# Kernel optimization log

Measured on AMD Instinct MI355X. Metric: run time of the kernel, lower is better.

## Reference

```python
import jax, jax.numpy as jnp
import numpy as np

B, D = 200000, 128
K = 1024


def setup_inputs() -> dict:
    key = jax.random.key(0)
    k1, k2 = jax.random.split(key)
    x_BD = jax.random.normal(k1, (B, D), dtype=jnp.float32)
    codebook = jax.random.uniform(k2, (K, D), dtype=jnp.float32)
    return {"x_BD": x_BD, "codebook": codebook}


def reference(x_BD, codebook):
    x_sq_B1 = jnp.sum(x_BD * x_BD, axis=-1, keepdims=True)
    c_sq_K = jnp.sum(codebook * codebook, axis=-1)
    dists_BK = x_sq_B1 - 2.0 * jnp.einsum("bd,kd->bk", x_BD, codebook) + c_sq_K
    codes_B = jnp.argmin(dists_BK, axis=-1)  # [B] int
    quant_x_BD = codebook[codes_B]           # gather, [B, D]
    return quant_x_BD, codes_B
```

## Files before the change

### kernel.cpp

```cpp
#include <hip/hip_runtime.h>


typedef float v2f __attribute__((ext_vector_type(2)));

#define DDIM 128
#define KCODES 1024
#define BM 64
#define BN 128
#define DCH 32
#define NTILES (KCODES / BN)
#define NCHUNK (DDIM / DCH)

__global__ void csq_kernel(const float* __restrict__ cb, float* __restrict__ csq) {
    int k = blockIdx.x * blockDim.x + threadIdx.x;
    if (k >= KCODES) return;
    const float* __restrict__ c = cb + (long)k * DDIM;
    float s0 = 0.f, s1 = 0.f, s2 = 0.f, s3 = 0.f;
#pragma unroll
    for (int d = 0; d < DDIM; d += 4) {
        s0 = fmaf(c[d + 0], c[d + 0], s0);
        s1 = fmaf(c[d + 1], c[d + 1], s1);
        s2 = fmaf(c[d + 2], c[d + 2], s2);
        s3 = fmaf(c[d + 3], c[d + 3], s3);
    }
    csq[k] = (s0 + s1) + (s2 + s3);
}

__launch_bounds__(256, 3)
__global__ void vq_gemm_kernel(const float* __restrict__ x, const float* __restrict__ cb,
                               const float* __restrict__ csq, float* __restrict__ quant,
                               float* __restrict__ codes) {
    __shared__ float xs[DDIM * BM];
    __shared__ float cs[DCH * BN];
    __shared__ int win[BM];

    const int tid = threadIdx.x;
    const long r0 = (long)blockIdx.x * BM;

    {
        const int r = tid >> 2;
        const int qb = (tid & 3) * 8;
        const float* __restrict__ xrow = x + (r0 + r) * DDIM;
#pragma unroll
        for (int j = 0; j < 8; ++j) {
            const int q = qb + j;
            const float4 v = *(const float4*)(xrow + q * 4);
            xs[(q * 4 + 0) * BM + r] = v.x;
            xs[(q * 4 + 1) * BM + r] = v.y;
            xs[(q * 4 + 2) * BM + r] = v.z;
            xs[(q * 4 + 3) * BM + r] = v.w;
        }
    }
    __syncthreads();

    const int tr = tid >> 4;
    const int tc = tid & 15;

    float s[4][4];
#pragma unroll
    for (int a = 0; a < 4; ++a)
#pragma unroll
        for (int b = 0; b < 4; ++b) s[a][b] = 0.f;
#pragma unroll
    for (int d = 0; d < DDIM; d += 4) {
#pragma unroll
        for (int dd = 0; dd < 4; ++dd) {
            const float4 v = *(const float4*)&xs[(d + dd) * BM + tr * 4];
            s[dd][0] = fmaf(v.x, v.x, s[dd][0]);
            s[dd][1] = fmaf(v.y, v.y, s[dd][1]);
            s[dd][2] = fmaf(v.z, v.z, s[dd][2]);
            s[dd][3] = fmaf(v.w, v.w, s[dd][3]);
        }
    }
    float xsq[4];
#pragma unroll
    for (int i = 0; i < 4; ++i) xsq[i] = (s[0][i] + s[1][i]) + (s[2][i] + s[3][i]);

    float best[4];
    int bidx[4];
#pragma unroll
    for (int i = 0; i < 4; ++i) { best[i] = 3.4e38f; bidx[i] = 0; }

    for (int ct = 0; ct < NTILES; ++ct) {
        v2f acc[4][4];
#pragma unroll
        for (int i = 0; i < 4; ++i)
#pragma unroll
            for (int jj = 0; jj < 4; ++jj) acc[i][jj] = (v2f){0.f, 0.f};

        for (int dc = 0; dc < NCHUNK; ++dc) {
            __syncthreads();
            {
                const int k = tid >> 1;
                const int qb = (tid & 1) * 4;
                const float* __restrict__ crow =
                    cb + (long)(ct * BN + k) * DDIM + dc * DCH;
#pragma unroll
                for (int j = 0; j < 4; ++j) {
                    const int q = qb + j;
                    const float4 v = *(const float4*)(crow + q * 4);
                    cs[(q * 4 + 0) * BN + k] = v.x;
                    cs[(q * 4 + 1) * BN + k] = v.y;
                    cs[(q * 4 + 2) * BN + k] = v.z;
                    cs[(q * 4 + 3) * BN + k] = v.w;
                }
            }
            __syncthreads();
#pragma unroll
            for (int d = 0; d < DCH; ++d) {
                const float4 xa  = *(const float4*)&xs[(dc * DCH + d) * BM + tr * 4];
                const float4 ca  = *(const float4*)&cs[d * BN + tc * 4];
                const float4 cb2 = *(const float4*)&cs[d * BN + 64 + tc * 4];
                const float xv[4] = {xa.x, xa.y, xa.z, xa.w};
                v2f cv[4];
                cv[0] = (v2f){ca.x, ca.y};
                cv[1] = (v2f){ca.z, ca.w};
                cv[2] = (v2f){cb2.x, cb2.y};
                cv[3] = (v2f){cb2.z, cb2.w};
#pragma unroll
                for (int i = 0; i < 4; ++i) {
                    const v2f xb = (v2f){xv[i], xv[i]};
#pragma unroll
                    for (int jj = 0; jj < 4; ++jj)
                        acc[i][jj] = __builtin_elementwise_fma(xb, cv[jj], acc[i][jj]);
                }
            }
        }

        float csq_r[8];
#pragma unroll
        for (int j = 0; j < 4; ++j) {
            csq_r[j]     = csq[ct * BN + tc * 4 + j];
            csq_r[4 + j] = csq[ct * BN + 64 + tc * 4 + j];
        }
#pragma unroll
        for (int i = 0; i < 4; ++i) {
#pragma unroll
            for (int jj = 0; jj < 4; ++jj) {
#pragma unroll
                for (int h = 0; h < 2; ++h) {
                    const int jl = jj * 2 + h;
                    const int cj = ct * BN + ((jl < 4) ? (tc * 4 + jl) : (64 + tc * 4 + jl - 4));
                    const float dist = fmaf(-2.0f, acc[i][jj][h], xsq[i]) + csq_r[jl];
                    if (dist < best[i]) { best[i] = dist; bidx[i] = cj; }
                }
            }
        }
    }

    __syncthreads();
    float* redb = cs;
    int* redi = (int*)cs + BM * 16;
#pragma unroll
    for (int i = 0; i < 4; ++i) {
        const int r = tr * 4 + i;
        redb[r * 16 + tc] = best[i];
        redi[r * 16 + tc] = bidx[i];
    }
    __syncthreads();
    if (tid < BM) {
        float b = redb[tid * 16];
        int bi = redi[tid * 16];
#pragma unroll
        for (int e = 1; e < 16; ++e) {
            const float v = redb[tid * 16 + e];
            const int vi = redi[tid * 16 + e];
            if (v < b || (v == b && vi < bi)) { b = v; bi = vi; }
        }
        codes[r0 + tid] = (float)bi;
        win[tid] = bi;
    }
    __syncthreads();

    {
        const int r = tid >> 2;
        const int qb = (tid & 3) * 8;
        const float* __restrict__ crow = cb + (long)win[r] * DDIM;
        float* __restrict__ qrow = quant + (r0 + r) * DDIM;
#pragma unroll
        for (int j = 0; j < 8; ++j) {
            const int q = qb + j;
            *(float4*)(qrow + q * 4) = *(const float4*)(crow + q * 4);
        }
    }
}

extern "C" void kernel_launch(void* const* d_in, const int* in_sizes, int n_in,
                              void* d_out, int out_size, void* d_ws, size_t ws_size,
                              hipStream_t stream) {
    const float* x  = (const float*)d_in[0];
    const float* cb = (const float*)d_in[1];
    const int B = in_sizes[0] / DDIM;

    float* quant = (float*)d_out;
    float* codes = (float*)d_out + (size_t)B * DDIM;
    float* csq   = (float*)d_ws;

    csq_kernel<<<(KCODES + 255) / 256, 256, 0, stream>>>(cb, csq);

    const int blocks = B / BM;
    vq_gemm_kernel<<<blocks, 256, 0, stream>>>(x, cb, csq, quant, codes);
}
```

Measured before the change: 815.5 us.

## Enlarge per-thread tile to 8x8 with packed FMA op_sel and shuffle argmin

Changes the codebook tile to 256 codes with 16-dim chunks and gives each thread an 8x8 output micro-tile. The inner loop uses inline v_pk_fma_f32 with op_sel to broadcast x lanes without repacking. The shared-memory argmin reduction is replaced by wavefront shuffles across 32 lanes. The aim is more FMAs per LDS load and fewer reduction syncs, at the cost of higher register pressure (64 accumulators) that may cut occupancy under the 3-blocks launch bound.

```diff
diff --git a/kernel.cpp b/kernel.cpp
--- a/kernel.cpp
+++ b/kernel.cpp
@@ -6,8 +6,8 @@
 #define DDIM 128
 #define KCODES 1024
 #define BM 64
-#define BN 128
-#define DCH 32
+#define BN 256
+#define DCH 16
 #define NTILES (KCODES / BN)
 #define NCHUNK (DDIM / DCH)
 
@@ -25,6 +25,13 @@
     }
     csq[k] = (s0 + s1) + (s2 + s3);
 }
+
+#define PK_LO(a, xx, cc) \
+    asm("v_pk_fma_f32 %0, %1, %2, %0 op_sel:[0,0,0] op_sel_hi:[0,1,1]" \
+        : "+v"(a) : "v"(xx), "v"(cc))
+#define PK_HI(a, xx, cc) \
+    asm("v_pk_fma_f32 %0, %1, %2, %0 op_sel:[1,0,0] op_sel_hi:[1,1,1]" \
+        : "+v"(a) : "v"(xx), "v"(cc))
 
 __launch_bounds__(256, 3)
 __global__ void vq_gemm_kernel(const float* __restrict__ x, const float* __restrict__ cb,
@@ -53,76 +60,84 @@
     }
     __syncthreads();
 
-    const int tr = tid >> 4;
-    const int tc = tid & 15;
-
-    float s[4][4];
+    const int tr = tid >> 5;
+    const int tc = tid & 31;
+
+    float s[4][8];
 #pragma unroll
     for (int a = 0; a < 4; ++a)
 #pragma unroll
-        for (int b = 0; b < 4; ++b) s[a][b] = 0.f;
+        for (int b = 0; b < 8; ++b) s[a][b] = 0.f;
 #pragma unroll
     for (int d = 0; d < DDIM; d += 4) {
 #pragma unroll
         for (int dd = 0; dd < 4; ++dd) {
-            const float4 v = *(const float4*)&xs[(d + dd) * BM + tr * 4];
-            s[dd][0] = fmaf(v.x, v.x, s[dd][0]);
-            s[dd][1] = fmaf(v.y, v.y, s[dd][1]);
-            s[dd][2] = fmaf(v.z, v.z, s[dd][2]);
-            s[dd][3] = fmaf(v.w, v.w, s[dd][3]);
-        }
-    }
-    float xsq[4];
-#pragma unroll
-    for (int i = 0; i < 4; ++i) xsq[i] = (s[0][i] + s[1][i]) + (s[2][i] + s[3][i]);
-
-    float best[4];
-    int bidx[4];
-#pragma unroll
-    for (int i = 0; i < 4; ++i) { best[i] = 3.4e38f; bidx[i] = 0; }
-
+            const float4 a0 = *(const float4*)&xs[(d + dd) * BM + tr * 8];
+            const float4 a1 = *(const float4*)&xs[(d + dd) * BM + tr * 8 + 4];
+            s[dd][0] = fmaf(a0.x, a0.x, s[dd][0]);
+            s[dd][1] = fmaf(a0.y, a0.y, s[dd][1]);
+            s[dd][2] = fmaf(a0.z, a0.z, s[dd][2]);
+            s[dd][3] = fmaf(a0.w, a0.w, s[dd][3]);
+            s[dd][4] = fmaf(a1.x, a1.x, s[dd][4]);
+            s[dd][5] = fmaf(a1.y, a1.y, s[dd][5]);
+            s[dd][6] = fmaf(a1.z, a1.z, s[dd][6]);
+            s[dd][7] = fmaf(a1.w, a1.w, s[dd][7]);
+        }
+    }
+    float xsq[8];
+#pragma unroll
+    for (int i = 0; i < 8; ++i) xsq[i] = (s[0][i] + s[1][i]) + (s[2][i] + s[3][i]);
+
+    float best[8];
+    int bidx[8];
+#pragma unroll
+    for (int i = 0; i < 8; ++i) { best[i] = 3.4e38f; bidx[i] = 0; }
+
+#pragma unroll 1
     for (int ct = 0; ct < NTILES; ++ct) {
-        v2f acc[4][4];
-#pragma unroll
-        for (int i = 0; i < 4; ++i)
+        v2f acc[8][4];
+#pragma unroll
+        for (int i = 0; i < 8; ++i)
 #pragma unroll
             for (int jj = 0; jj < 4; ++jj) acc[i][jj] = (v2f){0.f, 0.f};
 
+#pragma unroll 1
         for (int dc = 0; dc < NCHUNK; ++dc) {
             __syncthreads();
             {
-                const int k = tid >> 1;
-                const int qb = (tid & 1) * 4;
                 const float* __restrict__ crow =
-                    cb + (long)(ct * BN + k) * DDIM + dc * DCH;
+                    cb + (long)(ct * BN + tid) * DDIM + dc * DCH;
 #pragma unroll
                 for (int j = 0; j < 4; ++j) {
-                    const int q = qb + j;
-                    const float4 v = *(const float4*)(crow + q * 4);
-                    cs[(q * 4 + 0) * BN + k] = v.x;
-                    cs[(q * 4 + 1) * BN + k] = v.y;
-                    cs[(q * 4 + 2) * BN + k] = v.z;
-                    cs[(q * 4 + 3) * BN + k] = v.w;
+                    const float4 v = *(const float4*)(crow + j * 4);
+                    cs[(j * 4 + 0) * BN + tid] = v.x;
+                    cs[(j * 4 + 1) * BN + tid] = v.y;
+                    cs[(j * 4 + 2) * BN + tid] = v.z;
+                    cs[(j * 4 + 3) * BN + tid] = v.w;
                 }
             }
             __syncthreads();
 #pragma unroll
             for (int d = 0; d < DCH; ++d) {
-                const float4 xa  = *(const float4*)&xs[(dc * DCH + d) * BM + tr * 4];
-                const float4 ca  = *(const float4*)&cs[d * BN + tc * 4];
-                const float4 cb2 = *(const float4*)&cs[d * BN + 64 + tc * 4];
-                const float xv[4] = {xa.x, xa.y, xa.z, xa.w};
-                v2f cv[4];
-                cv[0] = (v2f){ca.x, ca.y};
-                cv[1] = (v2f){ca.z, ca.w};
-                cv[2] = (v2f){cb2.x, cb2.y};
-                cv[3] = (v2f){cb2.z, cb2.w};
-#pragma unroll
-                for (int i = 0; i < 4; ++i) {
-                    const v2f xb = (v2f){xv[i], xv[i]};
-#pragma unroll
-                    for (int jj = 0; jj < 4; ++jj)
-                        acc[i][jj] = __builtin_elementwise_fma(xb, cv[jj], acc[i][jj]);
+                const float4 xa0 = *(const float4*)&xs[(dc * DCH + d) * BM + tr * 8];
+                const float4 xa1 = *(const float4*)&xs[(dc * DCH + d) * BM + tr * 8 + 4];
+                const float4 ca0 = *(const float4*)&cs[d * BN + tc * 4];
+                const float4 ca1 = *(const float4*)&cs[d * BN + 128 + tc * 4];
+                v2f xp[4], cp[4];
+                xp[0] = (v2f){xa0.x, xa0.y}; xp[1] = (v2f){xa0.z, xa0.w};
+                xp[2] = (v2f){xa1.x, xa1.y}; xp[3] = (v2f){xa1.z, xa1.w};
+                cp[0] = (v2f){ca0.x, ca0.y}; cp[1] = (v2f){ca0.z, ca0.w};
+                cp[2] = (v2f){ca1.x, ca1.y}; cp[3] = (v2f){ca1.z, ca1.w};
+#pragma unroll
+                for (int jj = 0; jj < 4; ++jj) {
+                    PK_LO(acc[0][jj], xp[0], cp[jj]);
+                    PK_HI(acc[1][jj], xp[0], cp[jj]);
+                    PK_LO(acc[2][jj], xp[1], cp[jj]);
+                    PK_HI(acc[3][jj], xp[1], cp[jj]);
+                    PK_LO(acc[4][jj], xp[2], cp[jj]);
+                    PK_HI(acc[5][jj], xp[2], cp[jj]);
+                    PK_LO(acc[6][jj], xp[3], cp[jj]);
+                    PK_HI(acc[7][jj], xp[3], cp[jj]);
                 }
             }
         }
@@ -131,16 +146,16 @@
 #pragma unroll
         for (int j = 0; j < 4; ++j) {
             csq_r[j]     = csq[ct * BN + tc * 4 + j];
-            csq_r[4 + j] = csq[ct * BN + 64 + tc * 4 + j];
-        }
-#pragma unroll
-        for (int i = 0; i < 4; ++i) {
+            csq_r[4 + j] = csq[ct * BN + 128 + tc * 4 + j];
+        }
+#pragma unroll
+        for (int i = 0; i < 8; ++i) {
 #pragma unroll
             for (int jj = 0; jj < 4; ++jj) {
 #pragma unroll
                 for (int h = 0; h < 2; ++h) {
                     const int jl = jj * 2 + h;
-                    const int cj = ct * BN + ((jl < 4) ? (tc * 4 + jl) : (64 + tc * 4 + jl - 4));
+                    const int cj = ct * BN + ((jl < 4) ? (tc * 4 + jl) : (128 + tc * 4 + jl - 4));
                     const float dist = fmaf(-2.0f, acc[i][jj][h], xsq[i]) + csq_r[jl];
                     if (dist < best[i]) { best[i] = dist; bidx[i] = cj; }
                 }
@@ -148,27 +163,24 @@
         }
     }
 
-    __syncthreads();
-    float* redb = cs;
-    int* redi = (int*)cs + BM * 16;
-#pragma unroll
-    for (int i = 0; i < 4; ++i) {
-        const int r = tr * 4 + i;
-        redb[r * 16 + tc] = best[i];
-        redi[r * 16 + tc] = bidx[i];
-    }
-    __syncthreads();
-    if (tid < BM) {
-        float b = redb[tid * 16];
-        int bi = redi[tid * 16];
-#pragma unroll
-        for (int e = 1; e < 16; ++e) {
-            const float v = redb[tid * 16 + e];
-            const int vi = redi[tid * 16 + e];
-            if (v < b || (v == b && vi < bi)) { b = v; bi = vi; }
-        }
-        codes[r0 + tid] = (float)bi;
-        win[tid] = bi;
+#pragma unroll
+    for (int i = 0; i < 8; ++i) {
+#pragma unroll
+        for (int off = 16; off >= 1; off >>= 1) {
+            const float ov = __shfl_xor(best[i], off);
+            const int ovi = __shfl_xor(bidx[i], off);
+            if (ov < best[i] || (ov == best[i] && ovi < bidx[i])) {
+                best[i] = ov; bidx[i] = ovi;
+            }
+        }
+    }
+    if (tc == 0) {
+#pragma unroll
+        for (int i = 0; i < 8; ++i) {
+            const int r = tr * 8 + i;
+            codes[r0 + r] = (float)bidx[i];
+            win[r] = bidx[i];
+        }
     }
     __syncthreads();
 
```

Result: faster. 791.2 us (-3.0%).

## Use split-fp16 MFMA distance GEMM with exact fp32 recheck of ambiguous rows

Applied to the files above, without the earlier changes.

Replaces the fp32 FMA tiled GEMM with MFMA f16 matrix instructions. Both operands are split into high and low fp16 parts (three products: hi*hi, hi*lo, lo*hi) to approximate fp32 accuracy. The main kernel tracks the best and second-best distance per row and appends rows whose margin is below an error threshold to a global list via atomics. A follow-up kernel recomputes those rows exactly in fp32. This trades exact fp32 compute for matrix-core throughput, at the risk that the threshold heuristic misses near-ties or that many rows get rechecked.

```diff
diff --git a/kernel.cpp b/kernel.cpp
--- a/kernel.cpp
+++ b/kernel.cpp
@@ -1,17 +1,16 @@
 #include <hip/hip_runtime.h>
 
 
-typedef float v2f __attribute__((ext_vector_type(2)));
+typedef _Float16 f16;
+typedef f16 h8 __attribute__((ext_vector_type(8)));
+typedef float f4 __attribute__((ext_vector_type(4)));
 
 #define DDIM 128
 #define KCODES 1024
-#define BM 64
-#define BN 128
-#define DCH 32
-#define NTILES (KCODES / BN)
-#define NCHUNK (DDIM / DCH)
-
-__global__ void csq_kernel(const float* __restrict__ cb, float* __restrict__ csq) {
+
+__global__ void csq_kernel(const float* __restrict__ cb, float* __restrict__ csq,
+                           int* __restrict__ cnt) {
+    if (blockIdx.x == 0 && threadIdx.x == 0) *cnt = 0;
     int k = blockIdx.x * blockDim.x + threadIdx.x;
     if (k >= KCODES) return;
     const float* __restrict__ c = cb + (long)k * DDIM;
@@ -26,162 +25,195 @@
     csq[k] = (s0 + s1) + (s2 + s3);
 }
 
-__launch_bounds__(256, 3)
-__global__ void vq_gemm_kernel(const float* __restrict__ x, const float* __restrict__ cb,
+__global__ void bprep_kernel(const float* __restrict__ cb, h8* __restrict__ B2) {
+    const int t = blockIdx.x * 256 + threadIdx.x;
+    const int tile = t >> 6;
+    const int lane = t & 63;
+    const int cb16 = tile / 12, kf = tile % 12;
+    const int col = cb16 * 16 + (lane & 15);
+    const int kk0 = kf * 32 + (lane >> 4) * 8;
+    const int seg = kk0 >> 7;
+    const int kd0 = kk0 & 127;
+    const float* __restrict__ p = cb + (long)col * DDIM + kd0;
+    h8 out;
+#pragma unroll
+    for (int j = 0; j < 8; ++j) {
+        const float v = p[j];
+        const f16 h = (f16)v;
+        out[j] = (seg == 1) ? (f16)(v - (float)h) : h;
+    }
+    B2[tile * 64 + lane] = out;
+}
+
+__launch_bounds__(256)
+__global__ void vq_mfma_kernel(const float* __restrict__ x, const float* __restrict__ cb,
+                               const h8* __restrict__ B2, const float* __restrict__ csq,
+                               float* __restrict__ quant, float* __restrict__ codes,
+                               int* __restrict__ cnt, int* __restrict__ list) {
+    const int tid = threadIdx.x;
+    const int lane = tid & 63;
+    const int wv = tid >> 6;
+    const long gr0 = (long)blockIdx.x * 64 + (long)wv * 16;
+    const int lr = lane & 15;
+    const int lk = lane >> 4;
+
+    h8 ah[4], al[4];
+    float ss = 0.f;
+#pragma unroll
+    for (int f = 0; f < 4; ++f) {
+        const float* p = x + (gr0 + lr) * DDIM + f * 32 + lk * 8;
+        const float4 u0 = *(const float4*)p;
+        const float4 u1 = *(const float4*)(p + 4);
+        const float xv[8] = {u0.x, u0.y, u0.z, u0.w, u1.x, u1.y, u1.z, u1.w};
+#pragma unroll
+        for (int j = 0; j < 8; ++j) {
+            const float v = xv[j];
+            const f16 h = (f16)v;
+            ah[f][j] = h;
+            al[f][j] = (f16)(v - (float)h);
+            ss = fmaf(v, v, ss);
+        }
+    }
+    ss += __shfl_xor(ss, 16);
+    ss += __shfl_xor(ss, 32);
+    const float thr = 2.5e-3f * sqrtf(ss) + 0.04f;
+
+    float b1[4], b2v[4];
+    int i1[4];
+#pragma unroll
+    for (int r = 0; r < 4; ++r) { b1[r] = 3.4e38f; b2v[r] = 3.4e38f; i1[r] = 0; }
+
+#pragma unroll 1
+    for (int ct = 0; ct < 8; ++ct) {
+#pragma unroll 4
+        for (int cf = 0; cf < 8; ++cf) {
+            const int cb16 = ct * 8 + cf;
+            const h8* bp = B2 + cb16 * 12 * 64 + lane;
+            f4 acc = (f4){0.f, 0.f, 0.f, 0.f};
+#pragma unroll
+            for (int kf = 0; kf < 12; ++kf) {
+                const h8 bfrag = bp[kf * 64];
+                const h8 afrag = (kf < 4) ? ah[kf] : (kf < 8 ? ah[kf - 4] : al[kf - 8]);
+                acc = __builtin_amdgcn_mfma_f32_16x16x32_f16(afrag, bfrag, acc, 0, 0, 0);
+            }
+            const int col = ct * 128 + cf * 16 + lr;
+            const float cq = csq[col];
+#pragma unroll
+            for (int r = 0; r < 4; ++r) {
+                const float s = fmaf(-2.0f, acc[r], cq);
+                if (s < b1[r]) { b2v[r] = b1[r]; b1[r] = s; i1[r] = col; }
+                else if (s < b2v[r]) { b2v[r] = s; }
+            }
+        }
+    }
+
+#pragma unroll
+    for (int r = 0; r < 4; ++r) {
+#pragma unroll
+        for (int off = 1; off <= 8; off <<= 1) {
+            const float ob1 = __shfl_xor(b1[r], off);
+            const int   oi  = __shfl_xor(i1[r], off);
+            const float ob2 = __shfl_xor(b2v[r], off);
+            const bool ow = (ob1 < b1[r]) || (ob1 == b1[r] && oi < i1[r]);
+            const float nb2 = ow ? fminf(b1[r], ob2) : fminf(ob1, b2v[r]);
+            if (ow) { b1[r] = ob1; i1[r] = oi; }
+            b2v[r] = nb2;
+        }
+    }
+
+    float thrr[4];
+#pragma unroll
+    for (int r = 0; r < 4; ++r) thrr[r] = __shfl(thr, lk * 4 + r);
+
+    if (lr == 0) {
+#pragma unroll
+        for (int r = 0; r < 4; ++r) {
+            const long grow = gr0 + lk * 4 + r;
+            codes[grow] = (float)i1[r];
+            if (!(b2v[r] - b1[r] >= thrr[r])) {
+                const int pos = atomicAdd(cnt, 1);
+                list[pos] = (int)grow;
+            }
+        }
+    }
+
+    {
+        const int m = lane >> 2;
+        const int src = (m >> 2) * 16;
+        const int w0 = __shfl(i1[0], src), w1 = __shfl(i1[1], src);
+        const int w2 = __shfl(i1[2], src), w3 = __shfl(i1[3], src);
+        const int rs = m & 3;
+        const int win = rs == 0 ? w0 : rs == 1 ? w1 : rs == 2 ? w2 : w3;
+        const float* __restrict__ crow = cb + (long)win * DDIM + (lane & 3) * 32;
+        float* __restrict__ qrow = quant + (gr0 + m) * DDIM + (lane & 3) * 32;
+#pragma unroll
+        for (int q = 0; q < 8; ++q)
+            *(float4*)(qrow + q * 4) = *(const float4*)(crow + q * 4);
+    }
+}
+
+__launch_bounds__(256)
+__global__ void recheck_kernel(const float* __restrict__ x, const float* __restrict__ cb,
                                const float* __restrict__ csq, float* __restrict__ quant,
-                               float* __restrict__ codes) {
-    __shared__ float xs[DDIM * BM];
-    __shared__ float cs[DCH * BN];
-    __shared__ int win[BM];
-
-    const int tid = threadIdx.x;
-    const long r0 = (long)blockIdx.x * BM;
-
-    {
-        const int r = tid >> 2;
-        const int qb = (tid & 3) * 8;
-        const float* __restrict__ xrow = x + (r0 + r) * DDIM;
-#pragma unroll
-        for (int j = 0; j < 8; ++j) {
-            const int q = qb + j;
-            const float4 v = *(const float4*)(xrow + q * 4);
-            xs[(q * 4 + 0) * BM + r] = v.x;
-            xs[(q * 4 + 1) * BM + r] = v.y;
-            xs[(q * 4 + 2) * BM + r] = v.z;
-            xs[(q * 4 + 3) * BM + r] = v.w;
-        }
-    }
-    __syncthreads();
-
-    const int tr = tid >> 4;
-    const int tc = tid & 15;
-
-    float s[4][4];
-#pragma unroll
-    for (int a = 0; a < 4; ++a)
-#pragma unroll
-        for (int b = 0; b < 4; ++b) s[a][b] = 0.f;
-#pragma unroll
-    for (int d = 0; d < DDIM; d += 4) {
-#pragma unroll
-        for (int dd = 0; dd < 4; ++dd) {
-            const float4 v = *(const float4*)&xs[(d + dd) * BM + tr * 4];
-            s[dd][0] = fmaf(v.x, v.x, s[dd][0]);
-            s[dd][1] = fmaf(v.y, v.y, s[dd][1]);
-            s[dd][2] = fmaf(v.z, v.z, s[dd][2]);
-            s[dd][3] = fmaf(v.w, v.w, s[dd][3]);
-        }
-    }
-    float xsq[4];
-#pragma unroll
-    for (int i = 0; i < 4; ++i) xsq[i] = (s[0][i] + s[1][i]) + (s[2][i] + s[3][i]);
-
-    float best[4];
-    int bidx[4];
-#pragma unroll
-    for (int i = 0; i < 4; ++i) { best[i] = 3.4e38f; bidx[i] = 0; }
-
-    for (int ct = 0; ct < NTILES; ++ct) {
-        v2f acc[4][4];
-#pragma unroll
-        for (int i = 0; i < 4; ++i)
-#pragma unroll
-            for (int jj = 0; jj < 4; ++jj) acc[i][jj] = (v2f){0.f, 0.f};
-
-        for (int dc = 0; dc < NCHUNK; ++dc) {
-            __syncthreads();
-            {
-                const int k = tid >> 1;
-                const int qb = (tid & 1) * 4;
-                const float* __restrict__ crow =
-                    cb + (long)(ct * BN + k) * DDIM + dc * DCH;
-#pragma unroll
-                for (int j = 0; j < 4; ++j) {
-                    const int q = qb + j;
-                    const float4 v = *(const float4*)(crow + q * 4);
-                    cs[(q * 4 + 0) * BN + k] = v.x;
-                    cs[(q * 4 + 1) * BN + k] = v.y;
-                    cs[(q * 4 + 2) * BN + k] = v.z;
-                    cs[(q * 4 + 3) * BN + k] = v.w;
+                               float* __restrict__ codes, const int* __restrict__ cnt,
+                               const int* __restrict__ list) {
+    const int n = *cnt;
+    const int lane = threadIdx.x & 63;
+    const int wid = (blockIdx.x * 256 + threadIdx.x) >> 6;
+    const int nw = (gridDim.x * 256) >> 6;
+    for (int it = wid; it < n; it += nw) {
+        const int row = list[it];
+        const float* __restrict__ xr = x + (long)row * DDIM;
+        float accv[16];
+#pragma unroll
+        for (int t = 0; t < 16; ++t) accv[t] = 0.f;
+        float s4[4] = {0.f, 0.f, 0.f, 0.f};
+#pragma unroll 1
+        for (int d0 = 0; d0 < DDIM; d0 += 16) {
+            float xv[16];
+#pragma unroll
+            for (int q = 0; q < 4; ++q) {
+                const float4 u = *(const float4*)(xr + d0 + q * 4);
+                xv[q * 4 + 0] = u.x; xv[q * 4 + 1] = u.y;
+                xv[q * 4 + 2] = u.z; xv[q * 4 + 3] = u.w;
+            }
+#pragma unroll
+            for (int dd = 0; dd < 16; ++dd)
+                s4[dd & 3] = fmaf(xv[dd], xv[dd], s4[dd & 3]);
+#pragma unroll
+            for (int t = 0; t < 16; ++t) {
+                const float* __restrict__ cr = cb + (long)(lane + t * 64) * DDIM + d0;
+                float a = accv[t];
+#pragma unroll
+                for (int q = 0; q < 4; ++q) {
+                    const float4 c4 = *(const float4*)(cr + q * 4);
+                    a = fmaf(xv[q * 4 + 0], c4.x, a);
+                    a = fmaf(xv[q * 4 + 1], c4.y, a);
+                    a = fmaf(xv[q * 4 + 2], c4.z, a);
+                    a = fmaf(xv[q * 4 + 3], c4.w, a);
                 }
-            }
-            __syncthreads();
-#pragma unroll
-            for (int d = 0; d < DCH; ++d) {
-                const float4 xa  = *(const float4*)&xs[(dc * DCH + d) * BM + tr * 4];
-                const float4 ca  = *(const float4*)&cs[d * BN + tc * 4];
-                const float4 cb2 = *(const float4*)&cs[d * BN + 64 + tc * 4];
-                const float xv[4] = {xa.x, xa.y, xa.z, xa.w};
-                v2f cv[4];
-                cv[0] = (v2f){ca.x, ca.y};
-                cv[1] = (v2f){ca.z, ca.w};
-                cv[2] = (v2f){cb2.x, cb2.y};
-                cv[3] = (v2f){cb2.z, cb2.w};
-#pragma unroll
-                for (int i = 0; i < 4; ++i) {
-                    const v2f xb = (v2f){xv[i], xv[i]};
-#pragma unroll
-                    for (int jj = 0; jj < 4; ++jj)
-                        acc[i][jj] = __builtin_elementwise_fma(xb, cv[jj], acc[i][jj]);
-                }
-            }
-        }
-
-        float csq_r[8];
-#pragma unroll
-        for (int j = 0; j < 4; ++j) {
-            csq_r[j]     = csq[ct * BN + tc * 4 + j];
-            csq_r[4 + j] = csq[ct * BN + 64 + tc * 4 + j];
-        }
-#pragma unroll
-        for (int i = 0; i < 4; ++i) {
-#pragma unroll
-            for (int jj = 0; jj < 4; ++jj) {
-#pragma unroll
-                for (int h = 0; h < 2; ++h) {
-                    const int jl = jj * 2 + h;
-                    const int cj = ct * BN + ((jl < 4) ? (tc * 4 + jl) : (64 + tc * 4 + jl - 4));
-                    const float dist = fmaf(-2.0f, acc[i][jj][h], xsq[i]) + csq_r[jl];
-                    if (dist < best[i]) { best[i] = dist; bidx[i] = cj; }
-                }
-            }
-        }
-    }
-
-    __syncthreads();
-    float* redb = cs;
-    int* redi = (int*)cs + BM * 16;
-#pragma unroll
-    for (int i = 0; i < 4; ++i) {
-        const int r = tr * 4 + i;
-        redb[r * 16 + tc] = best[i];
-        redi[r * 16 + tc] = bidx[i];
-    }
-    __syncthreads();
-    if (tid < BM) {
-        float b = redb[tid * 16];
-        int bi = redi[tid * 16];
-#pragma unroll
-        for (int e = 1; e < 16; ++e) {
-            const float v = redb[tid * 16 + e];
-            const int vi = redi[tid * 16 + e];
-            if (v < b || (v == b && vi < bi)) { b = v; bi = vi; }
-        }
-        codes[r0 + tid] = (float)bi;
-        win[tid] = bi;
-    }
-    __syncthreads();
-
-    {
-        const int r = tid >> 2;
-        const int qb = (tid & 3) * 8;
-        const float* __restrict__ crow = cb + (long)win[r] * DDIM;
-        float* __restrict__ qrow = quant + (r0 + r) * DDIM;
-#pragma unroll
-        for (int j = 0; j < 8; ++j) {
-            const int q = qb + j;
-            *(float4*)(qrow + q * 4) = *(const float4*)(crow + q * 4);
-        }
+                accv[t] = a;
+            }
+        }
+        const float xsq = (s4[0] + s4[1]) + (s4[2] + s4[3]);
+        float b = 3.4e38f; int bi = 0;
+#pragma unroll
+        for (int t = 0; t < 16; ++t) {
+            const int k = lane + t * 64;
+            const float dist = fmaf(-2.0f, accv[t], xsq) + csq[k];
+            if (dist < b) { b = dist; bi = k; }
+        }
+#pragma unroll
+        for (int off = 32; off >= 1; off >>= 1) {
+            const float ov = __shfl_xor(b, off);
+            const int oi = __shfl_xor(bi, off);
+            if (ov < b || (ov == b && oi < bi)) { b = ov; bi = oi; }
+        }
+        if (lane == 0) codes[row] = (float)bi;
+        const float* __restrict__ crow = cb + (long)bi * DDIM + lane * 2;
+        float* __restrict__ qrow = quant + (long)row * DDIM + lane * 2;
+        qrow[0] = crow[0];
+        qrow[1] = crow[1];
     }
 }
 
@@ -194,10 +226,15 @@
 
     float* quant = (float*)d_out;
     float* codes = (float*)d_out + (size_t)B * DDIM;
-    float* csq   = (float*)d_ws;
-
-    csq_kernel<<<(KCODES + 255) / 256, 256, 0, stream>>>(cb, csq);
-
-    const int blocks = B / BM;
-    vq_gemm_kernel<<<blocks, 256, 0, stream>>>(x, cb, csq, quant, codes);
-}
+
+    char* ws = (char*)d_ws;
+    float* csq = (float*)ws;
+    int*   cnt = (int*)(ws + 4096);
+    h8*    B2  = (h8*)(ws + 8192);
+    int*   list = (int*)(ws + 8192 + 786432);
+
+    csq_kernel<<<(KCODES + 255) / 256, 256, 0, stream>>>(cb, csq, cnt);
+    bprep_kernel<<<192, 256, 0, stream>>>(cb, B2);
+    vq_mfma_kernel<<<B / 64, 256, 0, stream>>>(x, cb, B2, csq, quant, codes, cnt, list);
+    recheck_kernel<<<256, 256, 0, stream>>>(x, cb, csq, quant, codes, cnt, list);
+}
```

Result: slower. 904.7 us (+10.9%).
